# Optimization experiments

Hardware: AMD Instinct MI355X
Metric: run time of the kernel (lower is better)

Reference implementation:

```python
import jax, jax.numpy as jnp
import numpy as np

V, E, H, L, B, T = 32000, 256, 512, 128, 16, 128


def _gru_scan(x_emb, h0, W_ih, b_ih, W_hh, b_hh):
    # x_emb: [T, B, E] time-major; torch GRU gate order (r, z, n)
    gx = jnp.einsum('tbe,ge->tbg', x_emb, W_ih) + b_ih  # [T, B, 3H]
    def step(h, g):
        gh = h @ W_hh.T + b_hh
        xr, xz, xn = jnp.split(g, 3, axis=-1)
        hr, hz, hn = jnp.split(gh, 3, axis=-1)
        r = jax.nn.sigmoid(xr + hr)
        u = jax.nn.sigmoid(xz + hz)
        n = jnp.tanh(xn + r * hn)
        h_new = (1.0 - u) * n + u * h
        return h_new, h_new
    return jax.lax.scan(step, h0, gx)


def setup_inputs() -> dict:
    key = jax.random.key(0)
    ks = jax.random.split(key, 20)
    s = 0.02
    f = lambda k, shp: jax.random.normal(k, shp, dtype=jnp.float32) * s
    return {
        'x': jax.random.randint(ks[0], (B, T), 0, V),
        'enc_emb': f(ks[1], (V, E)),
        'enc_W_ih': f(ks[2], (3 * H, E)),
        'enc_b_ih': f(ks[3], (3 * H,)),
        'enc_W_hh': f(ks[4], (3 * H, H)),
        'enc_b_hh': f(ks[5], (3 * H,)),
        'fc_enc_W': f(ks[6], (L, H)),
        'fc_enc_b': f(ks[7], (L,)),
        'fc_dec_W': f(ks[8], (H, L)),
        'fc_dec_b': f(ks[9], (H,)),
        'dec_emb': f(ks[10], (V, E)),
        'dec_W_ih': f(ks[11], (3 * H, E)),
        'dec_b_ih': f(ks[12], (3 * H,)),
        'dec_W_hh': f(ks[13], (3 * H, H)),
        'dec_b_hh': f(ks[14], (3 * H,)),
        'dec_fc_W': f(ks[15], (V, H)),
        'dec_fc_b': f(ks[16], (V,)),
    }


def reference(x, enc_emb, enc_W_ih, enc_b_ih, enc_W_hh, enc_b_hh,
              fc_enc_W, fc_enc_b, fc_dec_W, fc_dec_b,
              dec_emb, dec_W_ih, dec_b_ih, dec_W_hh, dec_b_hh,
              dec_fc_W, dec_fc_b):
    Bx, Tx = x.shape
    Hh = enc_W_hh.shape[1]
    # Encoder: GRU over full sequence, take final hidden
    xe = enc_emb[x].transpose(1, 0, 2)                    # [T, B, E]
    h_last, _ = _gru_scan(xe, jnp.zeros((Bx, Hh), xe.dtype),
                          enc_W_ih, enc_b_ih, enc_W_hh, enc_b_hh)
    z = h_last @ fc_enc_W.T + fc_enc_b                    # [B, L]
    hid0 = jnp.tanh(z @ fc_dec_W.T + fc_dec_b)            # [B, H]
    # Decoder with teacher_forcing=1.0: inputs are x[:, 0:T-1]
    de = dec_emb[x[:, :-1]].transpose(1, 0, 2)            # [T-1, B, E]
    _, hs = _gru_scan(de, hid0, dec_W_ih, dec_b_ih, dec_W_hh, dec_b_hh)
    logits = jnp.einsum('tbh,vh->btv', hs, dec_fc_W) + dec_fc_b  # [B, T-1, V]
    Vv = dec_fc_W.shape[0]
    outputs = jnp.zeros((Bx, Tx, Vv), logits.dtype).at[:, 1:].set(logits)
    return outputs, z
```

## Files before the change

kernel.cpp:

```cpp
#include <hip/hip_runtime.h>

#define Vv 32000
#define Ee 256
#define Hh 512
#define Ll 128
#define Bb 16
#define Tt 128
#define G3 1536
#define NSW 256
#define NPAIRB (Bb * Hh)

typedef __attribute__((ext_vector_type(8))) short short8;
typedef __attribute__((ext_vector_type(4))) float f32x4;

__device__ __forceinline__ float sigmoidf_(float x) { return 1.f / (1.f + __expf(-x)); }

__device__ __forceinline__ unsigned short f2bf(float f) {
  unsigned int u = __float_as_uint(f);
  u = (u + 0x7fffu + ((u >> 16) & 1u)) >> 16;
  return (unsigned short)u;
}

__device__ __forceinline__ void transpose_body(int b, const float* __restrict__ in,
                                               float* __restrict__ outp) {
  __shared__ float tile[32][33];
  int bx = b & 7, by = b >> 3;
  int tx = threadIdx.x & 31, ty = threadIdx.x >> 5;
  int c = bx * 32 + tx;
  int r0 = by * 32;
  for (int i = ty; i < 32; i += 8)
    tile[i][tx] = in[(size_t)(r0 + i) * 256 + c];
  __syncthreads();
  int r = r0 + tx;
  int c0 = bx * 32;
  for (int i = ty; i < 32; i += 8)
    outp[(size_t)(c0 + i) * 1536 + r] = tile[tx][i];
}

__global__ void __launch_bounds__(256) k_prep(
    const float* __restrict__ cvt_in, unsigned short* __restrict__ cvt_out, int ncvt,
    float* __restrict__ out, uint2* __restrict__ pairs0,
    const float* __restrict__ encWih, float* __restrict__ wihT_e,
    const float* __restrict__ decWih, float* __restrict__ wihT_d) {
  int bid = blockIdx.x;
  const int tid = threadIdx.x;
  if (bid < ncvt) {
    int i = bid * 256 + tid;
    float4 v = ((const float4*)cvt_in)[i];
    ushort4 o;
    o.x = f2bf(v.x); o.y = f2bf(v.y); o.z = f2bf(v.z); o.w = f2bf(v.w);
    ((ushort4*)cvt_out)[i] = o;
    return;
  }
  bid -= ncvt;
  if (bid < 2000) {
    int idx = bid * 256 + tid;
    int b = idx / Vv, v = idx % Vv;
    out[(size_t)b * Tt * Vv + v] = 0.f;
    return;
  }
  bid -= 2000;
  if (bid < 64) {
    uint4 z = make_uint4(0u, 0u, 0u, 0u);
    ((uint4*)pairs0)[bid * 256 + tid] = z;
    return;
  }
  bid -= 64;
  if (bid < 384) transpose_body(bid, encWih, wihT_e);
  else transpose_body(bid - 384, decWih, wihT_d);
}

__device__ __forceinline__ void gx_body(int e, const int* __restrict__ x,
                                        const float* __restrict__ emb,
                                        const float* __restrict__ WihT,
                                        const float* __restrict__ b_ih,
                                        float* __restrict__ gx) {
  __shared__ float A[16][Ee];
  int mt = e / 6, gy = e % 6;
  int g = gy * 256 + threadIdx.x;
  for (int i = 0; i < 16; i++) {
    int tok = x[i * Tt + mt];
    A[i][threadIdx.x] = emb[(size_t)tok * Ee + threadIdx.x];
  }
  __syncthreads();
  float acc[16];
  float bg = b_ih[g];
#pragma unroll
  for (int i = 0; i < 16; i++) acc[i] = bg;
#pragma unroll 4
  for (int ee = 0; ee < Ee; ee++) {
    float w = WihT[(size_t)ee * G3 + g];
#pragma unroll
    for (int i = 0; i < 16; i++) acc[i] = fmaf(A[i][ee], w, acc[i]);
  }
#pragma unroll
  for (int i = 0; i < 16; i++)
    gx[(size_t)(mt * 16 + i) * G3 + g] = acc[i];
}

__global__ void k_gx(const int* __restrict__ x, const float* __restrict__ emb,
                     const float* __restrict__ WihT, const float* __restrict__ b_ih,
                     float* __restrict__ gx) {
  gx_body(blockIdx.x, x, emb, WihT, b_ih, gx);
}

template <bool HSEQ>
__device__ __forceinline__ void scan_body(
    const float* __restrict__ Whh, const float* __restrict__ bhh,
    const float* __restrict__ gx, uint2* __restrict__ pairs,
    unsigned short* __restrict__ hseq, int nsteps) {
  __shared__ float h_lds[Hh];
  const int tid = threadIdx.x;
  const int wg = blockIdx.x;
  const int g = wg >> 4;
  const int wgl = wg & 15;
  const int wave = tid >> 6;
  const int lane = tid & 63;
  const int cl = lane >> 3;
  const int ks = lane & 7;
  const int j = wgl * 32 + wave * 8 + cl;
  const bool gate = (ks == 0);

  float wr[64], wz[64], wn[64];
  {
    const float* R = Whh + (size_t)j * Hh + ks * 4;
    const float* Z = R + (size_t)Hh * Hh;
    const float* N = Z + (size_t)Hh * Hh;
#pragma unroll
    for (int q = 0; q < 16; ++q) {
      float4 a = *(const float4*)(R + q * 32);
      float4 b = *(const float4*)(Z + q * 32);
      float4 c = *(const float4*)(N + q * 32);
      wr[4*q] = a.x; wr[4*q+1] = a.y; wr[4*q+2] = a.z; wr[4*q+3] = a.w;
      wz[4*q] = b.x; wz[4*q+1] = b.y; wz[4*q+2] = b.z; wz[4*q+3] = b.w;
      wn[4*q] = c.x; wn[4*q+1] = c.y; wn[4*q+2] = c.z; wn[4*q+3] = c.w;
    }
  }
  float bhr = 0.f, bhz = 0.f, bhn = 0.f;
  if (gate) { bhr = bhh[j]; bhz = bhh[Hh + j]; bhn = bhh[2 * Hh + j]; }

  float xr = 0.f, xz = 0.f, xn = 0.f;
  if (gate) {
    const float* gp = gx + (size_t)g * G3 + j;
    xr = gp[0]; xz = gp[Hh]; xn = gp[2 * Hh];
  }

  for (int t = 0; t < nsteps; ++t) {
    {
      const uint4* pp =
          (const uint4*)(pairs + (size_t)(t & 1) * NPAIRB + (size_t)g * Hh) + tid;
      const unsigned ep = (unsigned)t;
      uint4 v;
      for (int it = 0; it < 200000; ++it) {
        asm volatile("global_load_dwordx4 %0, %1, off sc1\n\ts_waitcnt vmcnt(0)"
                     : "=v"(v) : "v"(pp) : "memory");
        if (v.y == ep && v.w == ep) break;
      }
      *(float2*)&h_lds[2 * tid] =
          make_float2(__uint_as_float(v.x), __uint_as_float(v.z));
    }
    __syncthreads();

    float aR = 0.f, aZ = 0.f, aN = 0.f;
    {
      const float* hb = h_lds + ks * 4;
#pragma unroll
      for (int q = 0; q < 16; ++q) {
        float4 hv = *(const float4*)(hb + q * 32);
        aR = fmaf(wr[4*q+0], hv.x, aR);
        aR = fmaf(wr[4*q+1], hv.y, aR);
        aR = fmaf(wr[4*q+2], hv.z, aR);
        aR = fmaf(wr[4*q+3], hv.w, aR);
        aZ = fmaf(wz[4*q+0], hv.x, aZ);
        aZ = fmaf(wz[4*q+1], hv.y, aZ);
        aZ = fmaf(wz[4*q+2], hv.z, aZ);
        aZ = fmaf(wz[4*q+3], hv.w, aZ);
        aN = fmaf(wn[4*q+0], hv.x, aN);
        aN = fmaf(wn[4*q+1], hv.y, aN);
        aN = fmaf(wn[4*q+2], hv.z, aN);
        aN = fmaf(wn[4*q+3], hv.w, aN);
      }
    }
    aR += __shfl_xor(aR, 1, 64); aR += __shfl_xor(aR, 2, 64); aR += __shfl_xor(aR, 4, 64);
    aZ += __shfl_xor(aZ, 1, 64); aZ += __shfl_xor(aZ, 2, 64); aZ += __shfl_xor(aZ, 4, 64);
    aN += __shfl_xor(aN, 1, 64); aN += __shfl_xor(aN, 2, 64); aN += __shfl_xor(aN, 4, 64);

    if (gate) {
      float r = sigmoidf_(xr + aR + bhr);
      float u = sigmoidf_(xz + aZ + bhz);
      float n = tanhf(xn + r * (aN + bhn));
      float hold = h_lds[j];
      float hnew = (1.f - u) * n + u * hold;
      uint2 pv = make_uint2(__float_as_uint(hnew), (unsigned)(t + 1));
      uint2* dst = pairs + (size_t)((t + 1) & 1) * NPAIRB + (size_t)g * Hh + j;
      asm volatile("global_store_dwordx2 %0, %1, off sc1" : : "v"(dst), "v"(pv) : "memory");
      if (HSEQ) hseq[((size_t)t * Bb + g) * Hh + j] = f2bf(hnew);
      if (t + 1 < nsteps) {
        const float* gp = gx + (size_t)((t + 1) * Bb + g) * G3 + j;
        xr = gp[0]; xz = gp[Hh]; xn = gp[2 * Hh];
      }
    }
    __syncthreads();
  }
}

__global__ void __launch_bounds__(256, 1) k_enc_fused(
    const float* __restrict__ Whh, const float* __restrict__ bhh,
    const float* __restrict__ gx_e, uint2* __restrict__ pairs,
    const int* __restrict__ x, const float* __restrict__ dec_emb,
    const float* __restrict__ wihT_d, const float* __restrict__ dec_bih,
    float* __restrict__ gx_d) {
  if (blockIdx.x < NSW)
    scan_body<false>(Whh, bhh, gx_e, pairs, (unsigned short*)nullptr, Tt);
  else
    gx_body(blockIdx.x - NSW, x, dec_emb, wihT_d, dec_bih, gx_d);
}

__global__ void __launch_bounds__(256, 1) k_dec_scan(
    const float* __restrict__ Whh, const float* __restrict__ bhh,
    const float* __restrict__ gx_d, uint2* __restrict__ pairs,
    unsigned short* __restrict__ hseq) {
  scan_body<true>(Whh, bhh, gx_d, pairs, hseq, Tt - 1);
}

__global__ void k_zh(const uint2* __restrict__ hp,
                     const float* __restrict__ Wz, const float* __restrict__ bz,
                     float* __restrict__ zout,
                     const float* __restrict__ Wh, const float* __restrict__ bh,
                     uint2* __restrict__ hp0) {
  int b = blockIdx.x;
  int tid = threadIdx.x;
  __shared__ float hsh[Hh];
  __shared__ float zsh[Ll];
  hsh[tid] = __uint_as_float(hp[b * Hh + tid].x);
  __syncthreads();
  if (tid < Ll) {
    float acc = bz[tid];
#pragma unroll 4
    for (int k = 0; k < Hh; k++) acc = fmaf(hsh[k], Wz[(size_t)tid * Hh + k], acc);
    zsh[tid] = acc;
    zout[b * Ll + tid] = acc;
  }
  __syncthreads();
  float acc = bh[tid];
#pragma unroll 4
  for (int l = 0; l < Ll; l++) acc = fmaf(zsh[l], Wh[(size_t)tid * Ll + l], acc);
  hp0[b * Hh + tid] = make_uint2(__float_as_uint(tanhf(acc)), 0u);
}

template <bool BF16W>
__global__ void __launch_bounds__(512, 1) k_logits_mfma(
    const unsigned short* __restrict__ Abf,
    const unsigned short* __restrict__ Wbf,
    const float* __restrict__ Wf,
    const float* __restrict__ bias, float* __restrict__ out) {
  __shared__ short W_lds[32768];
  const int tid = threadIdx.x;
  const int wave = tid >> 6, lane = tid & 63;
  const int ln = lane & 15, hi = lane >> 4;
  const int n0 = blockIdx.x * 64;

#pragma unroll
  for (int c = 0; c < 8; ++c) {
    int f = c * 512 + tid;
    int row = f & 63;
    int kc = f >> 6;
    short8 v;
    if (BF16W) {
      v = *(const short8*)(Wbf + (size_t)(n0 + row) * Hh + kc * 8);
    } else {
      const float* q = Wf + (size_t)(n0 + row) * Hh + kc * 8;
      short8 tv;
#pragma unroll
      for (int e = 0; e < 8; ++e) tv[e] = (short)f2bf(q[e]);
      v = tv;
    }
    *(short8*)&W_lds[f * 8] = v;
  }
  __syncthreads();

  f32x4 bv[4];
#pragma unroll
  for (int ni = 0; ni < 4; ++ni)
    bv[ni] = *(const f32x4*)&bias[n0 + ni * 16 + hi * 4];

  for (int pass = 0; pass < 4; ++pass) {
    const int m0 = pass * 512 + wave * 64;
    const unsigned short* hp = Abf + (size_t)(m0 + ln) * Hh + hi * 8;
    f32x4 acc[4][4];
#pragma unroll
    for (int mi = 0; mi < 4; ++mi)
#pragma unroll
      for (int ni = 0; ni < 4; ++ni) acc[mi][ni] = (f32x4)0.f;

    for (int kt = 0; kt < 16; ++kt) {
      short8 aW[4], bH[4];
#pragma unroll
      for (int ni = 0; ni < 4; ++ni)
        aW[ni] = *(const short8*)&W_lds[(((kt * 4 + hi) * 64) + ni * 16 + ln) * 8];
#pragma unroll
      for (int mi = 0; mi < 4; ++mi)
        bH[mi] = *(const short8*)(hp + (size_t)mi * 16 * Hh + kt * 32);
#pragma unroll
      for (int mi = 0; mi < 4; ++mi)
#pragma unroll
        for (int ni = 0; ni < 4; ++ni)
          acc[mi][ni] = __builtin_amdgcn_mfma_f32_16x16x32_bf16(aW[ni], bH[mi], acc[mi][ni], 0, 0, 0);
    }

#pragma unroll
    for (int ni = 0; ni < 4; ++ni) {
      const int n = n0 + ni * 16 + hi * 4;
#pragma unroll
      for (int mi = 0; mi < 4; ++mi) {
        int m = m0 + mi * 16 + ln;
        if (m < 2032) {
          int t = m >> 4, bb = m & 15;
          float* dst = out + ((size_t)(bb * Tt + 1 + t)) * Vv + n;
          f32x4 o = acc[mi][ni] + bv[ni];
          __builtin_nontemporal_store(o, (f32x4*)dst);
        }
      }
    }
  }
}

extern "C" void kernel_launch(void* const* d_in, const int* in_sizes, int n_in,
                              void* d_out, int out_size, void* d_ws, size_t ws_size,
                              hipStream_t stream) {
  const int* x = (const int*)d_in[0];
  const float* enc_emb = (const float*)d_in[1];
  const float* enc_Wih = (const float*)d_in[2];
  const float* enc_bih = (const float*)d_in[3];
  const float* enc_Whh = (const float*)d_in[4];
  const float* enc_bhh = (const float*)d_in[5];
  const float* fc_enc_W = (const float*)d_in[6];
  const float* fc_enc_b = (const float*)d_in[7];
  const float* fc_dec_W = (const float*)d_in[8];
  const float* fc_dec_b = (const float*)d_in[9];
  const float* dec_emb = (const float*)d_in[10];
  const float* dec_Wih = (const float*)d_in[11];
  const float* dec_bih = (const float*)d_in[12];
  const float* dec_Whh = (const float*)d_in[13];
  const float* dec_bhh = (const float*)d_in[14];
  const float* dec_fcW = (const float*)d_in[15];
  const float* dec_fcb = (const float*)d_in[16];
  float* out = (float*)d_out;

  float* ws = (float*)d_ws;
  size_t off = 0;
  float* wihT_e = ws + off; off += 393216;
  float* wihT_d = ws + off; off += 393216;
  float* gx_e = ws + off; off += 3145728;
  float* gx_d = ws + off; off += 3121152;
  uint2* enc_pairs = (uint2*)(ws + off); off += 4 * NPAIRB;
  uint2* dec_pairs = (uint2*)(ws + off); off += 4 * NPAIRB;
  unsigned short* hseq_bf = (unsigned short*)(ws + off); off += 524288;
  size_t wbf_elems = (size_t)Vv * Hh;
  bool use_wbf = (off + wbf_elems / 2) * sizeof(float) <= ws_size;
  unsigned short* wbf = (unsigned short*)(ws + off);

  int ncvt = use_wbf ? (int)(wbf_elems / 4 / 256) : 0;
  k_prep<<<ncvt + 2000 + 64 + 768, 256, 0, stream>>>(
      dec_fcW, wbf, ncvt, out, enc_pairs, enc_Wih, wihT_e, dec_Wih, wihT_d);

  k_gx<<<128 * 6, 256, 0, stream>>>(x, enc_emb, wihT_e, enc_bih, gx_e);

  k_enc_fused<<<NSW + 762, 256, 0, stream>>>(enc_Whh, enc_bhh, gx_e, enc_pairs,
                                             x, dec_emb, wihT_d, dec_bih, gx_d);

  k_zh<<<16, 512, 0, stream>>>(enc_pairs, fc_enc_W, fc_enc_b,
                               out + (size_t)Bb * Tt * Vv, fc_dec_W, fc_dec_b, dec_pairs);

  k_dec_scan<<<NSW, 256, 0, stream>>>(dec_Whh, dec_bhh, gx_d, dec_pairs, hseq_bf);

  if (use_wbf)
    k_logits_mfma<true><<<500, 512, 0, stream>>>(hseq_bf, wbf, dec_fcW, dec_fcb, out);
  else
    k_logits_mfma<false><<<500, 512, 0, stream>>>(hseq_bf, (unsigned short*)nullptr,
                                                  dec_fcW, dec_fcb, out);
}
```

Measured before the change: 690.6 us.

## Fuse decoder scan with logits GEMM via per-batch progress counters

New measurement: 772.3 us. 11.8% more time.

```diff
diff --git a/kernel.cpp b/kernel.cpp
--- a/kernel.cpp
+++ b/kernel.cpp
@@ -9,6 +9,7 @@
 #define G3 1536
 #define NSW 256
 #define NPAIRB (Bb * Hh)
+#define NLOG 500
 
 typedef __attribute__((ext_vector_type(8))) short short8;
 typedef __attribute__((ext_vector_type(4))) float f32x4;
@@ -39,7 +40,7 @@
 
 __global__ void __launch_bounds__(256) k_prep(
     const float* __restrict__ cvt_in, unsigned short* __restrict__ cvt_out, int ncvt,
-    float* __restrict__ out, uint2* __restrict__ pairs0,
+    float* __restrict__ out, uint2* __restrict__ pairs0, int* __restrict__ gcnt,
     const float* __restrict__ encWih, float* __restrict__ wihT_e,
     const float* __restrict__ decWih, float* __restrict__ wihT_d) {
   int bid = blockIdx.x;
@@ -66,6 +67,12 @@
     return;
   }
   bid -= 64;
+  if (bid < 1) {
+    uint4 z = make_uint4(0u, 0u, 0u, 0u);
+    ((uint4*)gcnt)[tid] = z;
+    return;
+  }
+  bid -= 1;
   if (bid < 384) transpose_body(bid, encWih, wihT_e);
   else transpose_body(bid - 384, decWih, wihT_d);
 }
@@ -108,8 +115,8 @@
 __device__ __forceinline__ void scan_body(
     const float* __restrict__ Whh, const float* __restrict__ bhh,
     const float* __restrict__ gx, uint2* __restrict__ pairs,
-    unsigned short* __restrict__ hseq, int nsteps) {
-  __shared__ float h_lds[Hh];
+    unsigned short* __restrict__ hseq, int nsteps,
+    float* __restrict__ h_lds, int* __restrict__ gcnt) {
   const int tid = threadIdx.x;
   const int wg = blockIdx.x;
   const int g = wg >> 4;
@@ -194,13 +201,24 @@
       uint2 pv = make_uint2(__float_as_uint(hnew), (unsigned)(t + 1));
       uint2* dst = pairs + (size_t)((t + 1) & 1) * NPAIRB + (size_t)g * Hh + j;
       asm volatile("global_store_dwordx2 %0, %1, off sc1" : : "v"(dst), "v"(pv) : "memory");
-      if (HSEQ) hseq[((size_t)t * Bb + g) * Hh + j] = f2bf(hnew);
+      if (HSEQ) {
+        unsigned short* hp = hseq + ((size_t)t * Bb + g) * Hh + j;
+        int hv = (int)f2bf(hnew);
+        asm volatile("global_store_short %0, %1, off sc1" : : "v"(hp), "v"(hv) : "memory");
+      }
       if (t + 1 < nsteps) {
         const float* gp = gx + (size_t)((t + 1) * Bb + g) * G3 + j;
         xr = gp[0]; xz = gp[Hh]; xn = gp[2 * Hh];
       }
     }
+    if (HSEQ && tid == 0)
+      __hip_atomic_fetch_add(gcnt + g * 64, 1, __ATOMIC_RELAXED, __HIP_MEMORY_SCOPE_AGENT);
     __syncthreads();
+  }
+  if (HSEQ) {
+    asm volatile("s_waitcnt vmcnt(0)" ::: "memory");
+    if (tid == 0)
+      __hip_atomic_fetch_add(gcnt + g * 64, 1, __ATOMIC_RELAXED, __HIP_MEMORY_SCOPE_AGENT);
   }
 }
 
@@ -210,17 +228,117 @@
     const int* __restrict__ x, const float* __restrict__ dec_emb,
     const float* __restrict__ wihT_d, const float* __restrict__ dec_bih,
     float* __restrict__ gx_d) {
+  __shared__ float h_lds_e[Hh];
   if (blockIdx.x < NSW)
-    scan_body<false>(Whh, bhh, gx_e, pairs, (unsigned short*)nullptr, Tt);
+    scan_body<false>(Whh, bhh, gx_e, pairs, (unsigned short*)nullptr, Tt,
+                     h_lds_e, (int*)nullptr);
   else
     gx_body(blockIdx.x - NSW, x, dec_emb, wihT_d, dec_bih, gx_d);
 }
 
-__global__ void __launch_bounds__(256, 1) k_dec_scan(
+template <bool BF16W>
+__device__ __forceinline__ void logits_gated(
+    int nb, const unsigned short* __restrict__ hseq,
+    const unsigned short* __restrict__ Wbf, const float* __restrict__ Wf,
+    const float* __restrict__ bias, const int* __restrict__ gcnt,
+    float* __restrict__ out, short* __restrict__ W_lds ) {
+  const int tid = threadIdx.x;
+  const int wave = tid >> 6, lane = tid & 63;
+  const int ln = lane & 15, hi = lane >> 4;
+  const int n0 = nb * 64;
+
+  f32x4 bv[4];
+#pragma unroll
+  for (int ni = 0; ni < 4; ++ni)
+    bv[ni] = *(const f32x4*)&bias[n0 + ni * 16 + hi * 4];
+
+  for (int pass = 0; pass < 8; ++pass) {
+    const int thr = (pass == 7) ? 16 * 128 : 16 * (pass * 16 + 17) + 15;
+    for (;;) {
+      int p = 0x7FFFFFFF;
+      if (tid < 16) {
+        const int* pa = gcnt + tid * 64;
+        asm volatile("global_load_dword %0, %1, off sc1\n\ts_waitcnt vmcnt(0)"
+                     : "=v"(p) : "v"(pa) : "memory");
+      }
+      if (__syncthreads_and(p >= thr)) break;
+      __builtin_amdgcn_s_sleep(32);
+    }
+
+    const int m0 = pass * 256 + wave * 64;
+    const unsigned short* hp = hseq + (size_t)(m0 + ln) * Hh + hi * 8;
+    f32x4 acc[4][4];
+#pragma unroll
+    for (int mi = 0; mi < 4; ++mi)
+#pragma unroll
+      for (int ni = 0; ni < 4; ++ni) acc[mi][ni] = (f32x4)0.f;
+
+    for (int half = 0; half < 2; ++half) {
+      __syncthreads();
+#pragma unroll
+      for (int c = 0; c < 8; ++c) {
+        int f = c * 256 + tid;
+        int row = f & 63;
+        int kc = (f >> 6) + half * 32;
+        short8 v;
+        if (BF16W) {
+          v = *(const short8*)(Wbf + (size_t)(n0 + row) * Hh + kc * 8);
+        } else {
+          const float* q = Wf + (size_t)(n0 + row) * Hh + kc * 8;
+          short8 tv;
+#pragma unroll
+          for (int e = 0; e < 8; ++e) tv[e] = (short)f2bf(q[e]);
+          v = tv;
+        }
+        *(short8*)&W_lds[f * 8] = v;
+      }
+      __syncthreads();
+      for (int kt = half * 8; kt < half * 8 + 8; ++kt) {
+        short8 aW[4], bH[4];
+#pragma unroll
+        for (int ni = 0; ni < 4; ++ni)
+          aW[ni] = *(const short8*)
+              &W_lds[((((kt - half * 8) * 4 + hi) * 64) + ni * 16 + ln) * 8];
+#pragma unroll
+        for (int mi = 0; mi < 4; ++mi)
+          bH[mi] = *(const short8*)(hp + (size_t)mi * 16 * Hh + kt * 32);
+#pragma unroll
+        for (int mi = 0; mi < 4; ++mi)
+#pragma unroll
+          for (int ni = 0; ni < 4; ++ni)
+            acc[mi][ni] = __builtin_amdgcn_mfma_f32_16x16x32_bf16(aW[ni], bH[mi], acc[mi][ni], 0, 0, 0);
+      }
+    }
+
+#pragma unroll
+    for (int ni = 0; ni < 4; ++ni) {
+      const int n = n0 + ni * 16 + hi * 4;
+#pragma unroll
+      for (int mi = 0; mi < 4; ++mi) {
+        int m = m0 + mi * 16 + ln;
+        if (m < 2032) {
+          int t = m >> 4, bb = m & 15;
+          float* dst = out + ((size_t)(bb * Tt + 1 + t)) * Vv + n;
+          f32x4 o = acc[mi][ni] + bv[ni];
+          __builtin_nontemporal_store(o, (f32x4*)dst);
+        }
+      }
+    }
+  }
+}
+
+template <bool BF16W>
+__global__ void __launch_bounds__(256) k_dec_logits(
     const float* __restrict__ Whh, const float* __restrict__ bhh,
     const float* __restrict__ gx_d, uint2* __restrict__ pairs,
-    unsigned short* __restrict__ hseq) {
-  scan_body<true>(Whh, bhh, gx_d, pairs, hseq, Tt - 1);
+    unsigned short* __restrict__ hseq, int* __restrict__ gcnt,
+    const unsigned short* __restrict__ Wbf, const float* __restrict__ Wf,
+    const float* __restrict__ bias, float* __restrict__ out) {
+  __shared__ short smem[16384];
+  if (blockIdx.x < NSW)
+    scan_body<true>(Whh, bhh, gx_d, pairs, hseq, Tt - 1, (float*)smem, gcnt);
+  else
+    logits_gated<BF16W>(blockIdx.x - NSW, hseq, Wbf, Wf, bias, gcnt, out, smem);
 }
 
 __global__ void k_zh(const uint2* __restrict__ hp,
@@ -246,83 +364,6 @@
 #pragma unroll 4
   for (int l = 0; l < Ll; l++) acc = fmaf(zsh[l], Wh[(size_t)tid * Ll + l], acc);
   hp0[b * Hh + tid] = make_uint2(__float_as_uint(tanhf(acc)), 0u);
-}
-
-template <bool BF16W>
-__global__ void __launch_bounds__(512, 1) k_logits_mfma(
-    const unsigned short* __restrict__ Abf,
-    const unsigned short* __restrict__ Wbf,
-    const float* __restrict__ Wf,
-    const float* __restrict__ bias, float* __restrict__ out) {
-  __shared__ short W_lds[32768];
-  const int tid = threadIdx.x;
-  const int wave = tid >> 6, lane = tid & 63;
-  const int ln = lane & 15, hi = lane >> 4;
-  const int n0 = blockIdx.x * 64;
-
-#pragma unroll
-  for (int c = 0; c < 8; ++c) {
-    int f = c * 512 + tid;
-    int row = f & 63;
-    int kc = f >> 6;
-    short8 v;
-    if (BF16W) {
-      v = *(const short8*)(Wbf + (size_t)(n0 + row) * Hh + kc * 8);
-    } else {
-      const float* q = Wf + (size_t)(n0 + row) * Hh + kc * 8;
-      short8 tv;
-#pragma unroll
-      for (int e = 0; e < 8; ++e) tv[e] = (short)f2bf(q[e]);
-      v = tv;
-    }
-    *(short8*)&W_lds[f * 8] = v;
-  }
-  __syncthreads();
-
-  f32x4 bv[4];
-#pragma unroll
-  for (int ni = 0; ni < 4; ++ni)
-    bv[ni] = *(const f32x4*)&bias[n0 + ni * 16 + hi * 4];
-
-  for (int pass = 0; pass < 4; ++pass) {
-    const int m0 = pass * 512 + wave * 64;
-    const unsigned short* hp = Abf + (size_t)(m0 + ln) * Hh + hi * 8;
-    f32x4 acc[4][4];
-#pragma unroll
-    for (int mi = 0; mi < 4; ++mi)
-#pragma unroll
-      for (int ni = 0; ni < 4; ++ni) acc[mi][ni] = (f32x4)0.f;
-
-    for (int kt = 0; kt < 16; ++kt) {
-      short8 aW[4], bH[4];
-#pragma unroll
-      for (int ni = 0; ni < 4; ++ni)
-        aW[ni] = *(const short8*)&W_lds[(((kt * 4 + hi) * 64) + ni * 16 + ln) * 8];
-#pragma unroll
-      for (int mi = 0; mi < 4; ++mi)
-        bH[mi] = *(const short8*)(hp + (size_t)mi * 16 * Hh + kt * 32);
-#pragma unroll
-      for (int mi = 0; mi < 4; ++mi)
-#pragma unroll
-        for (int ni = 0; ni < 4; ++ni)
-          acc[mi][ni] = __builtin_amdgcn_mfma_f32_16x16x32_bf16(aW[ni], bH[mi], acc[mi][ni], 0, 0, 0);
-    }
-
-#pragma unroll
-    for (int ni = 0; ni < 4; ++ni) {
-      const int n = n0 + ni * 16 + hi * 4;
-#pragma unroll
-      for (int mi = 0; mi < 4; ++mi) {
-        int m = m0 + mi * 16 + ln;
-        if (m < 2032) {
-          int t = m >> 4, bb = m & 15;
-          float* dst = out + ((size_t)(bb * Tt + 1 + t)) * Vv + n;
-          f32x4 o = acc[mi][ni] + bv[ni];
-          __builtin_nontemporal_store(o, (f32x4*)dst);
-        }
-      }
-    }
-  }
 }
 
 extern "C" void kernel_launch(void* const* d_in, const int* in_sizes, int n_in,
@@ -355,14 +396,15 @@
   float* gx_d = ws + off; off += 3121152;
   uint2* enc_pairs = (uint2*)(ws + off); off += 4 * NPAIRB;
   uint2* dec_pairs = (uint2*)(ws + off); off += 4 * NPAIRB;
+  int* gcnt = (int*)(ws + off); off += 1024;
   unsigned short* hseq_bf = (unsigned short*)(ws + off); off += 524288;
   size_t wbf_elems = (size_t)Vv * Hh;
   bool use_wbf = (off + wbf_elems / 2) * sizeof(float) <= ws_size;
   unsigned short* wbf = (unsigned short*)(ws + off);
 
   int ncvt = use_wbf ? (int)(wbf_elems / 4 / 256) : 0;
-  k_prep<<<ncvt + 2000 + 64 + 768, 256, 0, stream>>>(
-      dec_fcW, wbf, ncvt, out, enc_pairs, enc_Wih, wihT_e, dec_Wih, wihT_d);
+  k_prep<<<ncvt + 2000 + 64 + 1 + 768, 256, 0, stream>>>(
+      dec_fcW, wbf, ncvt, out, enc_pairs, gcnt, enc_Wih, wihT_e, dec_Wih, wihT_d);
 
   k_gx<<<128 * 6, 256, 0, stream>>>(x, enc_emb, wihT_e, enc_bih, gx_e);
 
@@ -372,11 +414,11 @@
   k_zh<<<16, 512, 0, stream>>>(enc_pairs, fc_enc_W, fc_enc_b,
                                out + (size_t)Bb * Tt * Vv, fc_dec_W, fc_dec_b, dec_pairs);
 
-  k_dec_scan<<<NSW, 256, 0, stream>>>(dec_Whh, dec_bhh, gx_d, dec_pairs, hseq_bf);
-
   if (use_wbf)
-    k_logits_mfma<true><<<500, 512, 0, stream>>>(hseq_bf, wbf, dec_fcW, dec_fcb, out);
+    k_dec_logits<true><<<NSW + NLOG, 256, 0, stream>>>(
+        dec_Whh, dec_bhh, gx_d, dec_pairs, hseq_bf, gcnt, wbf, dec_fcW, dec_fcb, out);
   else
-    k_logits_mfma<false><<<500, 512, 0, stream>>>(hseq_bf, (unsigned short*)nullptr,
-                                                  dec_fcW, dec_fcb, out);
-}
+    k_dec_logits<false><<<NSW + NLOG, 256, 0, stream>>>(
+        dec_Whh, dec_bhh, gx_d, dec_pairs, hseq_bf, gcnt,
+        (unsigned short*)nullptr, dec_fcW, dec_fcb, out);
+}
```
